# Performance work log

Hardware: AMD Instinct MI355X
Metric: run time of the kernel (lower is better)

The kernel has to match this reference:

```python
import jax, jax.numpy as jnp
import numpy as np

B, N, OBS, ACT = 4, 256, 40, 8
HEAD, DIM = 8, 32
T = HEAD * DIM


def setup_inputs() -> dict:
    key = jax.random.key(0)
    ks = jax.random.split(key, 10)
    x = jax.random.normal(ks[0], (B, N + 1, OBS), dtype=jnp.float32)
    # last row, col 0 carries the (float-encoded) target intersection index
    tgt = jax.random.randint(ks[1], (B,), 0, N)
    x = x.at[:, -1, 0].set(tgt.astype(jnp.float32))
    adj = jax.random.uniform(ks[2], (N, N), dtype=jnp.float32)
    s = 0.02
    return {
        "x": x,
        "adj": adj,
        "We1": jax.random.normal(ks[3], (OBS, T), dtype=jnp.float32) * s,
        "be1": jnp.zeros((T,), jnp.float32),
        "We2": jax.random.normal(ks[4], (T, T), dtype=jnp.float32) * s,
        "be2": jnp.zeros((T,), jnp.float32),
        "Wl": jax.random.normal(ks[5], (T, T), dtype=jnp.float32) * s,
        "bl": jnp.zeros((T,), jnp.float32),
        "Wn": jax.random.normal(ks[6], (T, T), dtype=jnp.float32) * s,
        "bn": jnp.zeros((T,), jnp.float32),
        "Wh": jax.random.normal(ks[7], (T, T), dtype=jnp.float32) * s,
        "bh": jnp.zeros((T,), jnp.float32),
        "Wa": jax.random.normal(ks[8], (DIM, ACT), dtype=jnp.float32) * s,
        "ba": jnp.zeros((ACT,), jnp.float32),
    }


def reference(x, adj, We1, be1, We2, be2, Wl, bl, Wn, bn, Wh, bh, Wa, ba):
    b, np1, _ = x.shape
    n = np1 - 1
    tgt = x[:, -1, 0].astype(jnp.int32)          # [B] target intersection ids
    obs = x[:, :-1, :]                            # [B,N,OBS]
    # obs_embed: Linear+ReLU twice
    emb = jax.nn.relu(obs @ We1 + be1)
    emb = jax.nn.relu(emb @ We2 + be2)            # [B,N,T]
    # tile then matmul by adjacency: result is adj @ emb, replicated along dim 1
    ne = jnp.einsum('mn,bnd->bmd', adj, emb)      # [B,N,T]
    ne = jnp.broadcast_to(ne[:, None], (b, n, n, T))  # [B,N,N,T] (tiled, as in torch)
    # agent heads: [B,N,H,1,D]
    ah = jax.nn.relu(emb @ Wl + bl).reshape(b, n, 1, DIM, HEAD).transpose(0, 1, 4, 2, 3)
    # neighbor heads: [B,N,H,N,D]
    nh = jax.nn.relu(ne @ Wn + bn).reshape(b, n, n, DIM, HEAD).transpose(0, 1, 4, 2, 3)
    # einsum 'ijklm,ijknm->ijklm' with l=1: elementwise over d, summed over n
    attn = ah * nh.sum(axis=3, keepdims=True)     # [B,N,H,1,D]
    attn = jax.nn.softmax(attn, axis=-1)
    hid = jax.nn.relu(ne @ Wh + bh).reshape(b, n, n, DIM, HEAD).transpose(0, 1, 4, 2, 3)
    out = attn * hid.sum(axis=3, keepdims=True)   # [B,N,H,1,D]
    out = out.mean(axis=2).reshape(b, n, DIM)     # mean over heads -> [B,N,D]
    g = out[jnp.arange(b), tgt]                   # gather per-batch target row [B,D]
    act = g @ Wa + ba                             # [B,ACT]
    return act
```

## Files before the change

kernel.cpp:

```cpp
#include <hip/hip_runtime.h>

#define Bsz 4
#define Nn  256
#define OBSD 40
#define ACTD 8
#define HEADS 8
#define DIMD 32
#define Td  256
#define R   4

#define FMA4(accr, s, wv) \
    (accr).x = fmaf((s), (wv).x, (accr).x); \
    (accr).y = fmaf((s), (wv).y, (accr).y); \
    (accr).z = fmaf((s), (wv).z, (accr).z); \
    (accr).w = fmaf((s), (wv).w, (accr).w)

__global__ __launch_bounds__(512, 1) void k_emb(
                      const float* __restrict__ x,
                      const float* __restrict__ We1, const float* __restrict__ be1,
                      const float* __restrict__ We2, const float* __restrict__ be2,
                      float* __restrict__ emb,
                      float* __restrict__ snh, float* __restrict__ shid) {
    int g = blockIdx.x;
    int t = threadIdx.x;
    int row0 = g * R;
    int b = row0 >> 8;
    int n0 = row0 & 255;
    if (g == 0)      { for (int i = t; i < Bsz * Td; i += 512) snh[i]  = 0.f; }
    else if (g == 1) { for (int i = t; i < Bsz * Td; i += 512) shid[i] = 0.f; }

    __shared__ float4 obs_t[OBSD];
    __shared__ float4 h1_t[Td];
    __shared__ float4 part[8][R][64];
    if (t < R * OBSD) {
        int r = t & (R - 1), k = t >> 2;
        ((float*)&obs_t[k])[r] = x[(b * (Nn + 1) + n0 + r) * OBSD + k];
    }
    __syncthreads();

    if (t < Td) {
        float bias1 = be1[t];
        float a1[R] = {bias1, bias1, bias1, bias1};
        float wbuf[8];
#pragma unroll
        for (int p = 0; p < 8; ++p) wbuf[p] = We1[p * Td + t];
#pragma unroll
        for (int k = 0; k < OBSD; ++k) {
            float w = wbuf[k & 7];
            if (k + 8 < OBSD) wbuf[k & 7] = We1[(k + 8) * Td + t];
            float4 ov = obs_t[k];
            a1[0] = fmaf(ov.x, w, a1[0]);
            a1[1] = fmaf(ov.y, w, a1[1]);
            a1[2] = fmaf(ov.z, w, a1[2]);
            a1[3] = fmaf(ov.w, w, a1[3]);
        }
        h1_t[t] = make_float4(fmaxf(a1[0], 0.f), fmaxf(a1[1], 0.f),
                              fmaxf(a1[2], 0.f), fmaxf(a1[3], 0.f));
    }
    __syncthreads();

    int wv = t >> 6, c = t & 63;
    {
        float4 a2[R] = {};
        float4 buf[8];
#pragma unroll
        for (int p = 0; p < 8; ++p)
            buf[p] = *(const float4*)(We2 + ((wv << 5) + p) * Td + 4 * c);
#pragma unroll
        for (int i = 0; i < 32; ++i) {
            int k = (wv << 5) + i;
            float4 wvv = buf[i & 7];
            if (i + 8 < 32)
                buf[i & 7] = *(const float4*)(We2 + (k + 8) * Td + 4 * c);
            float4 hv = h1_t[k];
            FMA4(a2[0], hv.x, wvv);
            FMA4(a2[1], hv.y, wvv);
            FMA4(a2[2], hv.z, wvv);
            FMA4(a2[3], hv.w, wvv);
        }
#pragma unroll
        for (int r = 0; r < R; ++r) part[wv][r][c] = a2[r];
    }
    __syncthreads();

    if (t < Td) {
        int c2 = t >> 2, j = t & 3;
#pragma unroll
        for (int r = 0; r < R; ++r) {
            float v = be2[t];
#pragma unroll
            for (int w2 = 0; w2 < 8; ++w2) v += ((const float*)&part[w2][r][c2])[j];
            emb[(row0 + r) * Td + t] = fmaxf(v, 0.f);
        }
    }
}

__global__ __launch_bounds__(512, 1) void k_fused(
                        const float* __restrict__ adj, const float* __restrict__ emb,
                        const float* __restrict__ Wn, const float* __restrict__ bn,
                        const float* __restrict__ Wh, const float* __restrict__ bh,
                        float* __restrict__ snh, float* __restrict__ shid) {
    int g = blockIdx.x, b = blockIdx.y;
    int t = threadIdx.x;
    int m0 = g * R;
    __shared__ float4 arow_t[Nn];
    __shared__ float4 nrow_t[Td];
    __shared__ float4 partN[8][R][64];
    __shared__ float4 partH[8][R][64];
    if (t < Td)
        arow_t[t] = make_float4(adj[(m0 + 0) * Nn + t], adj[(m0 + 1) * Nn + t],
                                adj[(m0 + 2) * Nn + t], adj[(m0 + 3) * Nn + t]);
    __syncthreads();

    int wv = t >> 6, c = t & 63;
    const float* eb = emb + b * Nn * Td;

    {
        float4 aN[R] = {};
        float4 buf[8];
#pragma unroll
        for (int p = 0; p < 8; ++p)
            buf[p] = *(const float4*)(eb + ((wv << 5) + p) * Td + 4 * c);
#pragma unroll
        for (int i = 0; i < 32; ++i) {
            int n = (wv << 5) + i;
            float4 ev = buf[i & 7];
            if (i + 8 < 32)
                buf[i & 7] = *(const float4*)(eb + (n + 8) * Td + 4 * c);
            float4 ar = arow_t[n];
            FMA4(aN[0], ar.x, ev);
            FMA4(aN[1], ar.y, ev);
            FMA4(aN[2], ar.z, ev);
            FMA4(aN[3], ar.w, ev);
        }
#pragma unroll
        for (int r = 0; r < R; ++r) partN[wv][r][c] = aN[r];
    }
    __syncthreads();
    if (t < Td) {
        int c2 = t >> 2, j = t & 3;
        float nr[R];
#pragma unroll
        for (int r = 0; r < R; ++r) {
            float v = 0.f;
#pragma unroll
            for (int w2 = 0; w2 < 8; ++w2) v += ((const float*)&partN[w2][r][c2])[j];
            nr[r] = v;
        }
        nrow_t[t] = make_float4(nr[0], nr[1], nr[2], nr[3]);
    }
    __syncthreads();

    {
        float4 sN[R] = {};
        float4 sH[R] = {};
        float4 bufN[4], bufH[4];
#pragma unroll
        for (int p = 0; p < 4; ++p) {
            int k = (wv << 5) + p;
            bufN[p] = *(const float4*)(Wn + k * Td + 4 * c);
            bufH[p] = *(const float4*)(Wh + k * Td + 4 * c);
        }
#pragma unroll
        for (int i = 0; i < 32; ++i) {
            int k = (wv << 5) + i;
            float4 wn4 = bufN[i & 3];
            float4 wh4 = bufH[i & 3];
            if (i + 4 < 32) {
                bufN[i & 3] = *(const float4*)(Wn + (k + 4) * Td + 4 * c);
                bufH[i & 3] = *(const float4*)(Wh + (k + 4) * Td + 4 * c);
            }
            float4 nv = nrow_t[k];
            FMA4(sN[0], nv.x, wn4);  FMA4(sH[0], nv.x, wh4);
            FMA4(sN[1], nv.y, wn4);  FMA4(sH[1], nv.y, wh4);
            FMA4(sN[2], nv.z, wn4);  FMA4(sH[2], nv.z, wh4);
            FMA4(sN[3], nv.w, wn4);  FMA4(sH[3], nv.w, wh4);
        }
#pragma unroll
        for (int r = 0; r < R; ++r) { partN[wv][r][c] = sN[r]; partH[wv][r][c] = sH[r]; }
    }
    __syncthreads();

    if (t < Td) {
        int c2 = t >> 2, j = t & 3;
        float bnt = bn[t], bht = bh[t];
        float rs1 = 0.f, rs2 = 0.f;
#pragma unroll
        for (int r = 0; r < R; ++r) {
            float v1 = bnt, v2 = bht;
#pragma unroll
            for (int w2 = 0; w2 < 8; ++w2) {
                v1 += ((const float*)&partN[w2][r][c2])[j];
                v2 += ((const float*)&partH[w2][r][c2])[j];
            }
            rs1 += fmaxf(v1, 0.f);
            rs2 += fmaxf(v2, 0.f);
        }
        atomicAdd(&snh[b * Td + t], rs1);
        atomicAdd(&shid[b * Td + t], rs2);
    }
}

__global__ __launch_bounds__(256, 1) void k_final(
                        const float* __restrict__ x, const float* __restrict__ emb,
                        const float* __restrict__ Wl, const float* __restrict__ bl,
                        const float* __restrict__ snh, const float* __restrict__ shid,
                        const float* __restrict__ Wa, const float* __restrict__ ba,
                        float* __restrict__ out) {
    int b = blockIdx.x;
    int t = threadIdx.x;
    int tgt = (int)x[(b * (Nn + 1) + Nn) * OBSD + 0];
    tgt = tgt < 0 ? 0 : (tgt > Nn - 1 ? Nn - 1 : tgt);
    __shared__ float erow[Td], lg[Td], p[Td], od[DIMD];
    __shared__ float4 partL[4][64];
    erow[t] = emb[(b * Nn + tgt) * Td + t];
    __syncthreads();

    int wv = t >> 6, c = t & 63;
    {
        float4 aL = {};
        float4 buf[8];
#pragma unroll
        for (int pp = 0; pp < 8; ++pp)
            buf[pp] = *(const float4*)(Wl + ((wv << 6) + pp) * Td + 4 * c);
#pragma unroll
        for (int i = 0; i < 64; ++i) {
            int k = (wv << 6) + i;
            float4 wlv = buf[i & 7];
            if (i + 8 < 64)
                buf[i & 7] = *(const float4*)(Wl + (k + 8) * Td + 4 * c);
            FMA4(aL, erow[k], wlv);
        }
        partL[wv][c] = aL;
    }
    __syncthreads();

    int c2 = t >> 2, j = t & 3;
    float acc = bl[t];
#pragma unroll
    for (int w2 = 0; w2 < 4; ++w2) acc += ((const float*)&partL[w2][c2])[j];
    float ah = fmaxf(acc, 0.f);
    lg[t] = ah * snh[b * Td + t];
    __syncthreads();
    int h = t & 7;
    float mx = -1e30f;
#pragma unroll
    for (int d = 0; d < DIMD; ++d) mx = fmaxf(mx, lg[d * HEADS + h]);
    float se = 0.f;
#pragma unroll
    for (int d = 0; d < DIMD; ++d) se += __expf(lg[d * HEADS + h] - mx);
    float attn = __expf(lg[t] - mx) / se;
    p[t] = attn * shid[b * Td + t];
    __syncthreads();
    if (t < DIMD) {
        float s = 0.f;
#pragma unroll
        for (int hh = 0; hh < HEADS; ++hh) s += p[t * HEADS + hh];
        od[t] = s * (1.f / HEADS);
    }
    __syncthreads();
    if (t < ACTD) {
        float s = ba[t];
#pragma unroll
        for (int d = 0; d < DIMD; ++d) s = fmaf(od[d], Wa[d * ACTD + t], s);
        out[b * ACTD + t] = s;
    }
}

extern "C" void kernel_launch(void* const* d_in, const int* in_sizes, int n_in,
                              void* d_out, int out_size, void* d_ws, size_t ws_size,
                              hipStream_t stream) {
    const float* x   = (const float*)d_in[0];
    const float* adj = (const float*)d_in[1];
    const float* We1 = (const float*)d_in[2];
    const float* be1 = (const float*)d_in[3];
    const float* We2 = (const float*)d_in[4];
    const float* be2 = (const float*)d_in[5];
    const float* Wl  = (const float*)d_in[6];
    const float* bl  = (const float*)d_in[7];
    const float* Wn  = (const float*)d_in[8];
    const float* bn  = (const float*)d_in[9];
    const float* Wh  = (const float*)d_in[10];
    const float* bh  = (const float*)d_in[11];
    const float* Wa  = (const float*)d_in[12];
    const float* ba  = (const float*)d_in[13];
    float* out = (float*)d_out;

    float* emb  = (float*)d_ws;
    float* snh  = emb + Bsz * Nn * Td;
    float* shid = snh + Bsz * Td;

    k_emb<<<dim3(Bsz * Nn / R), dim3(512), 0, stream>>>(x, We1, be1, We2, be2,
                                                        emb, snh, shid);
    k_fused<<<dim3(Nn / R, Bsz), dim3(512), 0, stream>>>(adj, emb, Wn, bn, Wh, bh,
                                                         snh, shid);
    k_final<<<dim3(Bsz), dim3(256), 0, stream>>>(x, emb, Wl, bl, snh, shid, Wa, ba, out);
}
```

Before: 100.7 us.

## Stage weight and embedding tiles into LDS via double-buffered async global_load_lds

Replaces the register-prefetch loops in all three kernels with tiles copied asynchronously from global memory straight into LDS using the global_load_lds builtin. Tiles are double-buffered: the next tile's copy is issued while the current one is consumed, with a block barrier after each tile. k_final also moves from 256 to 512 threads so eight waves share the Wl reduction. The aim is to overlap global loads with FMAs and cut register pressure. The cost is more barriers and a larger LDS footprint, and correctness depends on the async copies having completed at each barrier.

```diff
diff --git a/kernel.cpp b/kernel.cpp
--- a/kernel.cpp
+++ b/kernel.cpp
@@ -1,4 +1,5 @@
 #include <hip/hip_runtime.h>
+#include <cstdint>
 
 #define Bsz 4
 #define Nn  256
@@ -15,25 +16,51 @@
     (accr).z = fmaf((s), (wv).z, (accr).z); \
     (accr).w = fmaf((s), (wv).w, (accr).w)
 
+typedef __attribute__((address_space(3))) void       lds_void;
+typedef const __attribute__((address_space(1))) void glb_void;
+
+__device__ __forceinline__ void dma16(const float* gp, const float* lds_base) {
+    __builtin_amdgcn_global_load_lds(
+        (glb_void*)(uintptr_t)gp,
+        (lds_void*)(uint32_t)(uintptr_t)lds_base,
+        16, 0, 0);
+}
+
 __global__ __launch_bounds__(512, 1) void k_emb(
-                      const float* __restrict__ x,
-                      const float* __restrict__ We1, const float* __restrict__ be1,
-                      const float* __restrict__ We2, const float* __restrict__ be2,
-                      float* __restrict__ emb,
-                      float* __restrict__ snh, float* __restrict__ shid) {
-    int g = blockIdx.x;
-    int t = threadIdx.x;
+        const float* __restrict__ x,
+        const float* __restrict__ We1, const float* __restrict__ be1,
+        const float* __restrict__ We2, const float* __restrict__ be2,
+        float* __restrict__ emb,
+        float* __restrict__ snh, float* __restrict__ shid) {
+    int g = blockIdx.x, t = threadIdx.x;
+    int wv = t >> 6, c = t & 63;
     int row0 = g * R;
-    int b = row0 >> 8;
-    int n0 = row0 & 255;
+    int b = row0 >> 8, n0 = row0 & 255;
+
+    __shared__ float  stage[2][32][Td];
+    __shared__ float4 part[8][R][64];
+    __shared__ float4 obs_t[OBSD];
+    __shared__ float4 h1_t[Td];
+    float* partF = (float*)part;
+
+#pragma unroll
+    for (int i = 0; i < 4; ++i) {
+        int slot = wv * 4 + i;
+        dma16(We2 + slot * Td + 4 * c, &stage[0][slot][0]);
+    }
+#pragma unroll
+    for (int i = 0; i < 5; ++i) {
+        int r = wv * 5 + i;
+        if (r < OBSD) {
+            float* dst = (r < 32) ? &stage[1][r][0] : &partF[(r - 32) * Td];
+            dma16(We1 + r * Td + 4 * c, dst);
+        }
+    }
+
     if (g == 0)      { for (int i = t; i < Bsz * Td; i += 512) snh[i]  = 0.f; }
     else if (g == 1) { for (int i = t; i < Bsz * Td; i += 512) shid[i] = 0.f; }
-
-    __shared__ float4 obs_t[OBSD];
-    __shared__ float4 h1_t[Td];
-    __shared__ float4 part[8][R][64];
     if (t < R * OBSD) {
-        int r = t & (R - 1), k = t >> 2;
+        int r = t & 3, k = t >> 2;
         ((float*)&obs_t[k])[r] = x[(b * (Nn + 1) + n0 + r) * OBSD + k];
     }
     __syncthreads();
@@ -41,13 +68,9 @@
     if (t < Td) {
         float bias1 = be1[t];
         float a1[R] = {bias1, bias1, bias1, bias1};
-        float wbuf[8];
-#pragma unroll
-        for (int p = 0; p < 8; ++p) wbuf[p] = We1[p * Td + t];
 #pragma unroll
         for (int k = 0; k < OBSD; ++k) {
-            float w = wbuf[k & 7];
-            if (k + 8 < OBSD) wbuf[k & 7] = We1[(k + 8) * Td + t];
+            float w = (k < 32) ? stage[1][k][t] : partF[(k - 32) * Td + t];
             float4 ov = obs_t[k];
             a1[0] = fmaf(ov.x, w, a1[0]);
             a1[1] = fmaf(ov.y, w, a1[1]);
@@ -59,30 +82,34 @@
     }
     __syncthreads();
 
-    int wv = t >> 6, c = t & 63;
-    {
-        float4 a2[R] = {};
-        float4 buf[8];
-#pragma unroll
-        for (int p = 0; p < 8; ++p)
-            buf[p] = *(const float4*)(We2 + ((wv << 5) + p) * Td + 4 * c);
-#pragma unroll
-        for (int i = 0; i < 32; ++i) {
-            int k = (wv << 5) + i;
-            float4 wvv = buf[i & 7];
-            if (i + 8 < 32)
-                buf[i & 7] = *(const float4*)(We2 + (k + 8) * Td + 4 * c);
+    float4 a2[R] = {};
+    for (int tile = 0; tile < 8; ++tile) {
+        int buf = tile & 1;
+        if (tile + 1 < 8) {
+#pragma unroll
+            for (int i = 0; i < 4; ++i) {
+                int slot = wv * 4 + i;
+                dma16(We2 + ((tile + 1) * 32 + slot) * Td + 4 * c,
+                      &stage[buf ^ 1][slot][0]);
+            }
+        }
+#pragma unroll
+        for (int i = 0; i < 4; ++i) {
+            int slot = wv * 4 + i;
+            int k = tile * 32 + slot;
+            float4 wvv = *(const float4*)&stage[buf][slot][4 * c];
             float4 hv = h1_t[k];
             FMA4(a2[0], hv.x, wvv);
             FMA4(a2[1], hv.y, wvv);
             FMA4(a2[2], hv.z, wvv);
             FMA4(a2[3], hv.w, wvv);
         }
-#pragma unroll
-        for (int r = 0; r < R; ++r) part[wv][r][c] = a2[r];
-    }
-    __syncthreads();
-
+        __syncthreads();
+    }
+
+#pragma unroll
+    for (int r = 0; r < R; ++r) part[wv][r][c] = a2[r];
+    __syncthreads();
     if (t < Td) {
         int c2 = t >> 2, j = t & 3;
 #pragma unroll
@@ -96,45 +123,64 @@
 }
 
 __global__ __launch_bounds__(512, 1) void k_fused(
-                        const float* __restrict__ adj, const float* __restrict__ emb,
-                        const float* __restrict__ Wn, const float* __restrict__ bn,
-                        const float* __restrict__ Wh, const float* __restrict__ bh,
-                        float* __restrict__ snh, float* __restrict__ shid) {
+        const float* __restrict__ adj, const float* __restrict__ emb,
+        const float* __restrict__ Wn, const float* __restrict__ bn,
+        const float* __restrict__ Wh, const float* __restrict__ bh,
+        float* __restrict__ snh, float* __restrict__ shid) {
     int g = blockIdx.x, b = blockIdx.y;
     int t = threadIdx.x;
+    int wv = t >> 6, c = t & 63;
     int m0 = g * R;
+
+    __shared__ float  stage[2][32][Td];
     __shared__ float4 arow_t[Nn];
     __shared__ float4 nrow_t[Td];
     __shared__ float4 partN[8][R][64];
     __shared__ float4 partH[8][R][64];
+
+    const float* eb = emb + b * Nn * Td;
+
+#pragma unroll
+    for (int i = 0; i < 4; ++i) {
+        int slot = wv * 4 + i;
+        dma16(eb + slot * Td + 4 * c, &stage[0][slot][0]);
+    }
     if (t < Td)
         arow_t[t] = make_float4(adj[(m0 + 0) * Nn + t], adj[(m0 + 1) * Nn + t],
                                 adj[(m0 + 2) * Nn + t], adj[(m0 + 3) * Nn + t]);
     __syncthreads();
 
-    int wv = t >> 6, c = t & 63;
-    const float* eb = emb + b * Nn * Td;
-
-    {
-        float4 aN[R] = {};
-        float4 buf[8];
-#pragma unroll
-        for (int p = 0; p < 8; ++p)
-            buf[p] = *(const float4*)(eb + ((wv << 5) + p) * Td + 4 * c);
-#pragma unroll
-        for (int i = 0; i < 32; ++i) {
-            int n = (wv << 5) + i;
-            float4 ev = buf[i & 7];
-            if (i + 8 < 32)
-                buf[i & 7] = *(const float4*)(eb + (n + 8) * Td + 4 * c);
+    float4 aN[R] = {};
+    for (int tile = 0; tile < 8; ++tile) {
+        int buf = tile & 1;
+        if (tile + 1 < 8) {
+#pragma unroll
+            for (int i = 0; i < 4; ++i) {
+                int slot = wv * 4 + i;
+                dma16(eb + ((tile + 1) * 32 + slot) * Td + 4 * c,
+                      &stage[buf ^ 1][slot][0]);
+            }
+        }
+#pragma unroll
+        for (int i = 0; i < 4; ++i) {
+            int slot = wv * 4 + i;
+            int n = tile * 32 + slot;
+            float4 ev = *(const float4*)&stage[buf][slot][4 * c];
             float4 ar = arow_t[n];
             FMA4(aN[0], ar.x, ev);
             FMA4(aN[1], ar.y, ev);
             FMA4(aN[2], ar.z, ev);
             FMA4(aN[3], ar.w, ev);
         }
-#pragma unroll
-        for (int r = 0; r < R; ++r) partN[wv][r][c] = aN[r];
+        __syncthreads();
+    }
+#pragma unroll
+    for (int r = 0; r < R; ++r) partN[wv][r][c] = aN[r];
+#pragma unroll
+    for (int i = 0; i < 2; ++i) {
+        int kl = wv * 2 + i;
+        dma16(Wn + kl * Td + 4 * c, &stage[0][kl][0]);
+        dma16(Wh + kl * Td + 4 * c, &stage[0][16 + kl][0]);
     }
     __syncthreads();
     if (t < Td) {
@@ -151,34 +197,33 @@
     }
     __syncthreads();
 
-    {
-        float4 sN[R] = {};
-        float4 sH[R] = {};
-        float4 bufN[4], bufH[4];
-#pragma unroll
-        for (int p = 0; p < 4; ++p) {
-            int k = (wv << 5) + p;
-            bufN[p] = *(const float4*)(Wn + k * Td + 4 * c);
-            bufH[p] = *(const float4*)(Wh + k * Td + 4 * c);
-        }
-#pragma unroll
-        for (int i = 0; i < 32; ++i) {
-            int k = (wv << 5) + i;
-            float4 wn4 = bufN[i & 3];
-            float4 wh4 = bufH[i & 3];
-            if (i + 4 < 32) {
-                bufN[i & 3] = *(const float4*)(Wn + (k + 4) * Td + 4 * c);
-                bufH[i & 3] = *(const float4*)(Wh + (k + 4) * Td + 4 * c);
-            }
+    float4 sN[R] = {};
+    float4 sH[R] = {};
+    for (int tile = 0; tile < 16; ++tile) {
+        int buf = tile & 1;
+        if (tile + 1 < 16) {
+#pragma unroll
+            for (int i = 0; i < 2; ++i) {
+                int kl = wv * 2 + i, k = (tile + 1) * 16 + kl;
+                dma16(Wn + k * Td + 4 * c, &stage[buf ^ 1][kl][0]);
+                dma16(Wh + k * Td + 4 * c, &stage[buf ^ 1][16 + kl][0]);
+            }
+        }
+#pragma unroll
+        for (int i = 0; i < 2; ++i) {
+            int kl = wv * 2 + i, k = tile * 16 + kl;
+            float4 wn4 = *(const float4*)&stage[buf][kl][4 * c];
+            float4 wh4 = *(const float4*)&stage[buf][16 + kl][4 * c];
             float4 nv = nrow_t[k];
             FMA4(sN[0], nv.x, wn4);  FMA4(sH[0], nv.x, wh4);
             FMA4(sN[1], nv.y, wn4);  FMA4(sH[1], nv.y, wh4);
             FMA4(sN[2], nv.z, wn4);  FMA4(sH[2], nv.z, wh4);
             FMA4(sN[3], nv.w, wn4);  FMA4(sH[3], nv.w, wh4);
         }
-#pragma unroll
-        for (int r = 0; r < R; ++r) { partN[wv][r][c] = sN[r]; partH[wv][r][c] = sH[r]; }
-    }
+        __syncthreads();
+    }
+#pragma unroll
+    for (int r = 0; r < R; ++r) { partN[wv][r][c] = sN[r]; partH[wv][r][c] = sH[r]; }
     __syncthreads();
 
     if (t < Td) {
@@ -201,56 +246,71 @@
     }
 }
 
-__global__ __launch_bounds__(256, 1) void k_final(
-                        const float* __restrict__ x, const float* __restrict__ emb,
-                        const float* __restrict__ Wl, const float* __restrict__ bl,
-                        const float* __restrict__ snh, const float* __restrict__ shid,
-                        const float* __restrict__ Wa, const float* __restrict__ ba,
-                        float* __restrict__ out) {
+__global__ __launch_bounds__(512, 1) void k_final(
+        const float* __restrict__ x, const float* __restrict__ emb,
+        const float* __restrict__ Wl, const float* __restrict__ bl,
+        const float* __restrict__ snh, const float* __restrict__ shid,
+        const float* __restrict__ Wa, const float* __restrict__ ba,
+        float* __restrict__ out) {
     int b = blockIdx.x;
     int t = threadIdx.x;
+    int wv = t >> 6, c = t & 63;
+
+    __shared__ float  stage[2][32][Td];
+    __shared__ float4 partL[8][64];
+    __shared__ float erow[Td], lg[Td], p[Td], od[DIMD];
+
+#pragma unroll
+    for (int i = 0; i < 4; ++i) {
+        int slot = wv * 4 + i;
+        dma16(Wl + slot * Td + 4 * c, &stage[0][slot][0]);
+    }
     int tgt = (int)x[(b * (Nn + 1) + Nn) * OBSD + 0];
     tgt = tgt < 0 ? 0 : (tgt > Nn - 1 ? Nn - 1 : tgt);
-    __shared__ float erow[Td], lg[Td], p[Td], od[DIMD];
-    __shared__ float4 partL[4][64];
-    erow[t] = emb[(b * Nn + tgt) * Td + t];
-    __syncthreads();
-
-    int wv = t >> 6, c = t & 63;
-    {
-        float4 aL = {};
-        float4 buf[8];
-#pragma unroll
-        for (int pp = 0; pp < 8; ++pp)
-            buf[pp] = *(const float4*)(Wl + ((wv << 6) + pp) * Td + 4 * c);
-#pragma unroll
-        for (int i = 0; i < 64; ++i) {
-            int k = (wv << 6) + i;
-            float4 wlv = buf[i & 7];
-            if (i + 8 < 64)
-                buf[i & 7] = *(const float4*)(Wl + (k + 8) * Td + 4 * c);
+    if (t < Td) erow[t] = emb[(b * Nn + tgt) * Td + t];
+    __syncthreads();
+
+    float4 aL = {};
+    for (int tile = 0; tile < 8; ++tile) {
+        int buf = tile & 1;
+        if (tile + 1 < 8) {
+#pragma unroll
+            for (int i = 0; i < 4; ++i) {
+                int slot = wv * 4 + i;
+                dma16(Wl + ((tile + 1) * 32 + slot) * Td + 4 * c,
+                      &stage[buf ^ 1][slot][0]);
+            }
+        }
+#pragma unroll
+        for (int i = 0; i < 4; ++i) {
+            int slot = wv * 4 + i;
+            int k = tile * 32 + slot;
+            float4 wlv = *(const float4*)&stage[buf][slot][4 * c];
             FMA4(aL, erow[k], wlv);
         }
-        partL[wv][c] = aL;
-    }
-    __syncthreads();
-
-    int c2 = t >> 2, j = t & 3;
-    float acc = bl[t];
-#pragma unroll
-    for (int w2 = 0; w2 < 4; ++w2) acc += ((const float*)&partL[w2][c2])[j];
-    float ah = fmaxf(acc, 0.f);
-    lg[t] = ah * snh[b * Td + t];
-    __syncthreads();
-    int h = t & 7;
-    float mx = -1e30f;
-#pragma unroll
-    for (int d = 0; d < DIMD; ++d) mx = fmaxf(mx, lg[d * HEADS + h]);
-    float se = 0.f;
-#pragma unroll
-    for (int d = 0; d < DIMD; ++d) se += __expf(lg[d * HEADS + h] - mx);
-    float attn = __expf(lg[t] - mx) / se;
-    p[t] = attn * shid[b * Td + t];
+        __syncthreads();
+    }
+    partL[wv][c] = aL;
+    __syncthreads();
+
+    if (t < Td) {
+        int c2 = t >> 2, j = t & 3;
+        float acc = bl[t];
+#pragma unroll
+        for (int w2 = 0; w2 < 8; ++w2) acc += ((const float*)&partL[w2][c2])[j];
+        lg[t] = fmaxf(acc, 0.f) * snh[b * Td + t];
+    }
+    __syncthreads();
+    if (t < Td) {
+        int h = t & 7;
+        float mx = -1e30f;
+#pragma unroll
+        for (int d = 0; d < DIMD; ++d) mx = fmaxf(mx, lg[d * HEADS + h]);
+        float se = 0.f;
+#pragma unroll
+        for (int d = 0; d < DIMD; ++d) se += __expf(lg[d * HEADS + h] - mx);
+        p[t] = (__expf(lg[t] - mx) / se) * shid[b * Td + t];
+    }
     __syncthreads();
     if (t < DIMD) {
         float s = 0.f;
@@ -294,5 +354,6 @@
                                                         emb, snh, shid);
     k_fused<<<dim3(Nn / R, Bsz), dim3(512), 0, stream>>>(adj, emb, Wn, bn, Wh, bh,
                                                          snh, shid);
-    k_final<<<dim3(Bsz), dim3(256), 0, stream>>>(x, emb, Wl, bl, snh, shid, Wa, ba, out);
-}
+    k_final<<<dim3(Bsz), dim3(512), 0, stream>>>(x, emb, Wl, bl, snh, shid,
+                                                 Wa, ba, out);
+}
```

After: 116.4 us. 15.6% more time.
